# Performance work log

Measured on AMD Instinct MI355X. Metric: run time of the kernel, lower is better.

Reference implementation:

```python
import jax, jax.numpy as jnp
import numpy as np

N_CHEM = 100000
N_PROT = 20000
D = 128           # hidden_channels, also input feature dim (lazy SAGEConv)
E = 600000        # edges chem->protein (reverse relation uses flipped index)
EL = 200000       # label edges for decoder
L = 3             # SAGEConv layers


def setup_inputs() -> dict:
    key = jax.random.key(0)
    ks = jax.random.split(key, 11)
    inp = {
        'x_chem':    jax.random.normal(ks[0], (N_CHEM, D), jnp.float32),
        'x_protein': jax.random.normal(ks[1], (N_PROT, D), jnp.float32),
        # Wl/bl/Wr stacked over [layer, relation]; relation 0 = chem->protein (dst protein),
        # relation 1 = protein->chem (dst chem). PyG SAGEConv: lin_l has bias, lin_r does not.
        'Wl': jax.random.normal(ks[2], (L, 2, D, D), jnp.float32) * 0.05,
        'bl': jax.random.normal(ks[3], (L, 2, D), jnp.float32) * 0.05,
        'Wr': jax.random.normal(ks[4], (L, 2, D, D), jnp.float32) * 0.05,
        'Wd': jax.random.normal(ks[5], (1, 2 * D), jnp.float32) * 0.05,
        'bd': jax.random.normal(ks[6], (1,), jnp.float32) * 0.05,
        'src_idx': jax.random.randint(ks[7], (E,), 0, N_CHEM, jnp.int64),
        'dst_idx': jax.random.randint(ks[8], (E,), 0, N_PROT, jnp.int64),
        'row': jax.random.randint(ks[9], (EL,), 0, N_CHEM, jnp.int64),
        'col': jax.random.randint(ks[10], (EL,), 0, N_PROT, jnp.int64),
    }
    return inp


def _sage(x_src, x_dst, s_idx, d_idx, Wl, bl, Wr, n_dst):
    # PyG SAGEConv (aggr='mean'): lin_l(mean_j x_src[j]) + lin_r(x_dst)
    msg = x_src[s_idx]                                   # [E, D] gather
    agg = jax.ops.segment_sum(msg, d_idx, num_segments=n_dst)
    deg = jax.ops.segment_sum(jnp.ones((s_idx.shape[0],), x_src.dtype), d_idx,
                              num_segments=n_dst)
    mean = agg / jnp.clip(deg, 1.0)[:, None]
    return mean @ Wl.T + bl + x_dst @ Wr.T


def reference(x_chem, x_protein, Wl, bl, Wr, Wd, bd, src_idx, dst_idx, row, col):
    h_c, h_p = x_chem, x_protein
    for l in range(L):
        new_p = _sage(h_c, h_p, src_idx, dst_idx, Wl[l, 0], bl[l, 0], Wr[l, 0], N_PROT)
        new_c = _sage(h_p, h_c, dst_idx, src_idx, Wl[l, 1], bl[l, 1], Wr[l, 1], N_CHEM)
        h_c, h_p = jax.nn.relu(new_c), jax.nn.relu(new_p)
    # EdgeDecoder: gather + concat + linear -> flat scores
    x = jnp.concatenate([h_c[row], h_p[col]], axis=-1)   # [EL, 2D]
    z = (x @ Wd.T + bd).reshape(-1)                      # [EL]
    return (z, x)
```

## Files before the change

kernel.cpp:

```cpp
#include <hip/hip_runtime.h>

#define D128 128

typedef __attribute__((ext_vector_type(8))) short bf16x8;
typedef __attribute__((ext_vector_type(4))) float f32x4;
typedef unsigned short u16;
typedef unsigned int u32;

__device__ __forceinline__ u16 f2b(float f) {
  union { float f; u32 u; } x; x.f = f;
  u32 r = x.u + 0x7fffu + ((x.u >> 16) & 1u);
  return (u16)(r >> 16);
}
__device__ __forceinline__ float b2f(short s) {
  union { u32 u; float f; } x; x.u = ((u32)(unsigned short)s) << 16; return x.f;
}

#define GLD16(gp, lp) __builtin_amdgcn_global_load_lds( \
    (const __attribute__((address_space(1))) void*)(gp), \
    (__attribute__((address_space(3))) void*)(lp), 16, 0, 0)

__global__ __launch_bounds__(256) void cvt_deg_k(const float* __restrict__ xc, const float* __restrict__ xp,
                                                 const float* __restrict__ Wl, const float* __restrict__ Wr,
                                                 const int* __restrict__ src, const int* __restrict__ dst,
                                                 u16* __restrict__ B0, u16* __restrict__ Wcat,
                                                 int* __restrict__ deg, int NP, int NT, int E) {
  const int nqx = NT * 32;
  const int ncvt = nqx + 49152;
  const int TOT = ncvt + E;
  for (int i = blockIdx.x * 256 + threadIdx.x; i < TOT; i += gridDim.x * 256) {
    if (i < nqx) {
      const int r = i >> 5, c4 = (i & 31) << 2;
      const float* sp = (r < NP) ? &xp[(size_t)r * D128 + c4]
                                 : &xc[(size_t)(r - NP) * D128 + c4];
      float4 f = *(const float4*)sp;
      uint2 u;
      u.x = (u32)f2b(f.x) | ((u32)f2b(f.y) << 16);
      u.y = (u32)f2b(f.z) | ((u32)f2b(f.w) << 16);
      *(uint2*)&B0[(size_t)i * 4] = u;
    } else if (i < ncvt) {
      const int t = (i - nqx) * 4;
      const int slice = t >> 15, j = (t >> 8) & 127, k = t & 255;
      const float* sw = (k < 128) ? &Wl[(size_t)slice * 16384 + j * 128 + k]
                                  : &Wr[(size_t)slice * 16384 + j * 128 + (k - 128)];
      float4 f = *(const float4*)sw;
      uint2 u;
      u.x = (u32)f2b(f.x) | ((u32)f2b(f.y) << 16);
      u.y = (u32)f2b(f.z) | ((u32)f2b(f.w) << 16);
      *(uint2*)&Wcat[t] = u;
    } else {
      const int e = i - ncvt;
      atomicAdd(&deg[dst[e]], 1);
      atomicAdd(&deg[NP + src[e]], 1);
    }
  }
}

__global__ __launch_bounds__(256) void scan_k(const int* __restrict__ deg, int* __restrict__ offp, int NT) {
  __shared__ int sh[256];
  const int c = blockIdx.x;
  const int tid = threadIdx.x;
  int pre = 0;
  const int lim = c * 2048;
  for (int i = tid; i < lim; i += 256) pre += deg[i];
  sh[tid] = pre; __syncthreads();
#pragma unroll
  for (int o = 128; o > 0; o >>= 1) {
    if (tid < o) sh[tid] += sh[tid + o];
    __syncthreads();
  }
  const int base_pre = sh[0];
  __syncthreads();
  const int base = lim + tid * 8;
  int v[8]; int s = 0;
#pragma unroll
  for (int u = 0; u < 8; ++u) { int i = base + u; v[u] = (i < NT) ? deg[i] : 0; s += v[u]; }
  sh[tid] = s; __syncthreads();
#pragma unroll
  for (int o = 1; o < 256; o <<= 1) {
    int t = (tid >= o) ? sh[tid - o] : 0;
    __syncthreads();
    sh[tid] += t;
    __syncthreads();
  }
  int run = sh[tid] - s + base_pre;
#pragma unroll
  for (int u = 0; u < 8; ++u) { int i = base + u; if (i < NT) offp[i] = run; run += v[u]; }
}

__global__ __launch_bounds__(256) void fill_k(const int* __restrict__ src, const int* __restrict__ dst,
                                              const int* __restrict__ offp, int* cur, int* adj,
                                              int NP, int E) {
  int e = blockIdx.x * 256 + threadIdx.x;
  if (e >= E) return;
  const int s = src[e], d = dst[e];
  const int cn = NP + s;
  int pp = atomicAdd(&cur[d], 1);  adj[offp[d] + pp] = cn;
  int pc = atomicAdd(&cur[cn], 1); adj[offp[cn] + pc] = d;
}

__global__ __launch_bounds__(256) void agg_k(const u16* __restrict__ hcur, u16* __restrict__ hnext,
                                             const int* __restrict__ adj, const int* __restrict__ offp,
                                             const int* __restrict__ deg, int NT) {
  const int v = blockIdx.x * 16 + (threadIdx.x >> 4);
  if (v >= NT) return;
  const int l16 = threadIdx.x & 15;
  const int s = offp[v], cnt = deg[v];
  float ac[8] = {0.f, 0.f, 0.f, 0.f, 0.f, 0.f, 0.f, 0.f};
  int idx = (l16 < cnt) ? adj[s + l16] : 0;
  for (int n = 0; n < cnt; n += 16) {
    const int batch = (cnt - n < 16) ? (cnt - n) : 16;
    const int nrem = cnt - n - 16;
    const int idxn = (nrem > 0 && l16 < nrem) ? adj[s + n + 16 + l16] : 0;
    int j = 0;
    for (; j + 8 <= batch; j += 8) {
      int i0 = __shfl(idx, j, 16),     i1 = __shfl(idx, j + 1, 16);
      int i2 = __shfl(idx, j + 2, 16), i3 = __shfl(idx, j + 3, 16);
      int i4 = __shfl(idx, j + 4, 16), i5 = __shfl(idx, j + 5, 16);
      int i6 = __shfl(idx, j + 6, 16), i7 = __shfl(idx, j + 7, 16);
      bf16x8 r0 = *(const bf16x8*)&hcur[(size_t)i0 * D128 + l16 * 8];
      bf16x8 r1 = *(const bf16x8*)&hcur[(size_t)i1 * D128 + l16 * 8];
      bf16x8 r2 = *(const bf16x8*)&hcur[(size_t)i2 * D128 + l16 * 8];
      bf16x8 r3 = *(const bf16x8*)&hcur[(size_t)i3 * D128 + l16 * 8];
      bf16x8 r4 = *(const bf16x8*)&hcur[(size_t)i4 * D128 + l16 * 8];
      bf16x8 r5 = *(const bf16x8*)&hcur[(size_t)i5 * D128 + l16 * 8];
      bf16x8 r6 = *(const bf16x8*)&hcur[(size_t)i6 * D128 + l16 * 8];
      bf16x8 r7 = *(const bf16x8*)&hcur[(size_t)i7 * D128 + l16 * 8];
#pragma unroll
      for (int k = 0; k < 8; ++k)
        ac[k] += ((b2f(r0[k]) + b2f(r1[k])) + (b2f(r2[k]) + b2f(r3[k])))
               + ((b2f(r4[k]) + b2f(r5[k])) + (b2f(r6[k]) + b2f(r7[k])));
    }
    for (; j + 4 <= batch; j += 4) {
      int i0 = __shfl(idx, j, 16),     i1 = __shfl(idx, j + 1, 16);
      int i2 = __shfl(idx, j + 2, 16), i3 = __shfl(idx, j + 3, 16);
      bf16x8 r0 = *(const bf16x8*)&hcur[(size_t)i0 * D128 + l16 * 8];
      bf16x8 r1 = *(const bf16x8*)&hcur[(size_t)i1 * D128 + l16 * 8];
      bf16x8 r2 = *(const bf16x8*)&hcur[(size_t)i2 * D128 + l16 * 8];
      bf16x8 r3 = *(const bf16x8*)&hcur[(size_t)i3 * D128 + l16 * 8];
#pragma unroll
      for (int k = 0; k < 8; ++k)
        ac[k] += (b2f(r0[k]) + b2f(r1[k])) + (b2f(r2[k]) + b2f(r3[k]));
    }
    for (; j < batch; ++j) {
      int i0 = __shfl(idx, j, 16);
      bf16x8 r0 = *(const bf16x8*)&hcur[(size_t)i0 * D128 + l16 * 8];
#pragma unroll
      for (int k = 0; k < 8; ++k) ac[k] += b2f(r0[k]);
    }
    idx = idxn;
  }
  const float inv = (cnt > 0) ? 1.f / (float)cnt : 0.f;
  uint4 pk;
  pk.x = (u32)f2b(ac[0] * inv) | ((u32)f2b(ac[1] * inv) << 16);
  pk.y = (u32)f2b(ac[2] * inv) | ((u32)f2b(ac[3] * inv) << 16);
  pk.z = (u32)f2b(ac[4] * inv) | ((u32)f2b(ac[5] * inv) << 16);
  pk.w = (u32)f2b(ac[6] * inv) | ((u32)f2b(ac[7] * inv) << 16);
  *(uint4*)&hnext[(size_t)v * D128 + l16 * 8] = pk;
}

__global__ __launch_bounds__(256) void gemm_both_k(u16* __restrict__ hnext, const u16* __restrict__ hcur,
                                                   const u16* __restrict__ Wcat_l, const float* __restrict__ bl_l,
                                                   int NP, int NT, int tilesP) {
  __shared__ u16 As[128 * 64];
  __shared__ u16 Bs[128 * 64];
  const int t = blockIdx.x;
  const bool isP = t < tilesP;
  const int rbase = isP ? t * 128 : NP + (t - tilesP) * 128;
  const int hi = isP ? NP : NT;
  const u16* __restrict__ W = Wcat_l + (isP ? 0 : 32768);
  const float* __restrict__ bias = bl_l + (isP ? 0 : 128);

  const int tid = threadIdx.x;
  const int w = tid >> 6, lane = tid & 63;
  const int wr = w >> 1, wc = w & 1;
  const int l15 = lane & 15, chi = lane >> 4;

  f32x4 acc[4][4];
#pragma unroll
  for (int m = 0; m < 4; ++m)
#pragma unroll
    for (int n = 0; n < 4; ++n) acc[m][n] = (f32x4){0.f, 0.f, 0.f, 0.f};

  for (int ks = 0; ks < 4; ++ks) {
    const int k0 = ks * 64;
    const u16* Xsrc = (k0 < 128) ? hnext : hcur;
    const int kb = k0 & 127;
    if (ks) __syncthreads();
#pragma unroll
    for (int q = 0; q < 4; ++q) {
      const int ibase = w * 256 + q * 64;
      const int i = ibase + lane;
      const int r = i >> 3;
      const int cg = (i & 7) ^ (r & 7);
      int rr = rbase + r; if (rr >= hi) rr = hi - 1;
      GLD16(Xsrc + (size_t)rr * D128 + kb + cg * 8, (char*)As + ibase * 16);
      GLD16(W + (size_t)r * 256 + k0 + cg * 8, (char*)Bs + ibase * 16);
    }
    __syncthreads();
#pragma unroll
    for (int kk = 0; kk < 2; ++kk) {
      bf16x8 a[4], bfr[4];
      const int c = kk * 4 + chi;
#pragma unroll
      for (int m = 0; m < 4; ++m) {
        const int r = wr * 64 + m * 16 + l15;
        a[m] = *(const bf16x8*)((const char*)As + (r * 8 + (c ^ (r & 7))) * 16);
      }
#pragma unroll
      for (int n = 0; n < 4; ++n) {
        const int j = wc * 64 + n * 16 + l15;
        bfr[n] = *(const bf16x8*)((const char*)Bs + (j * 8 + (c ^ (j & 7))) * 16);
      }
#pragma unroll
      for (int m = 0; m < 4; ++m)
#pragma unroll
        for (int n = 0; n < 4; ++n)
          acc[m][n] = __builtin_amdgcn_mfma_f32_16x16x32_bf16(a[m], bfr[n], acc[m][n], 0, 0, 0);
    }
  }
#pragma unroll
  for (int n = 0; n < 4; ++n) {
    const int col = wc * 64 + n * 16 + l15;
    const float bv = bias[col];
#pragma unroll
    for (int m = 0; m < 4; ++m) {
      const int rb2 = rbase + wr * 64 + m * 16 + chi * 4;
#pragma unroll
      for (int q = 0; q < 4; ++q) {
        const int row = rb2 + q;
        if (row < hi) {
          float vv = acc[m][n][q] + bv;
          vv = vv > 0.f ? vv : 0.f;
          hnext[(size_t)row * D128 + col] = f2b(vv);
        }
      }
    }
  }
}

__global__ __launch_bounds__(256) void decoder_k(const u16* __restrict__ hf,
                                                 const int* __restrict__ rowi, const int* __restrict__ coli,
                                                 const float* __restrict__ Wd, const float* __restrict__ bd,
                                                 float* __restrict__ out, int NP, int EL) {
  typedef __attribute__((ext_vector_type(8))) unsigned short u16x8;
  const int lane = threadIdx.x & 63;
  const int half = lane >> 5;
  const int l32 = lane & 31;
  const int wid = blockIdx.x * 4 + (threadIdx.x >> 6);
  const int nw = gridDim.x * 4;
  float wvv[8];
#pragma unroll
  for (int k = 0; k < 8; ++k) wvv[k] = Wd[l32 * 8 + k];
  const float bdv = bd[0];
  for (int e = wid * 2 + half; e < EL; e += nw * 2) {
    const int r = rowi[e], c = coli[e];
    const size_t hrow = (l32 < 16) ? ((size_t)(NP + r) * D128 + l32 * 8)
                                   : ((size_t)c * D128 + (l32 - 16) * 8);
    const u16x8 hb = *(const u16x8*)&hf[hrow];
    float x0 = b2f((short)hb[0]), x1 = b2f((short)hb[1]);
    float x2 = b2f((short)hb[2]), x3 = b2f((short)hb[3]);
    float x4 = b2f((short)hb[4]), x5 = b2f((short)hb[5]);
    float x6 = b2f((short)hb[6]), x7 = b2f((short)hb[7]);
    float p = x0 * wvv[0] + x1 * wvv[1] + x2 * wvv[2] + x3 * wvv[3]
            + x4 * wvv[4] + x5 * wvv[5] + x6 * wvv[6] + x7 * wvv[7];
#pragma unroll
    for (int m = 1; m < 32; m <<= 1) p += __shfl_xor(p, m, 64);
    float* xo = out + (size_t)EL + (size_t)e * 256 + l32 * 8;
    f32x4 lo = {x0, x1, x2, x3};
    f32x4 hi2 = {x4, x5, x6, x7};
    __builtin_nontemporal_store(lo, (f32x4*)xo);
    __builtin_nontemporal_store(hi2, (f32x4*)(xo + 4));
    if (l32 == 0) __builtin_nontemporal_store(p + bdv, &out[e]);
  }
}


extern "C" void kernel_launch(void* const* d_in, const int* in_sizes, int n_in,
                              void* d_out, int out_size, void* d_ws, size_t ws_size,
                              hipStream_t stream) {
  const float* x_chem = (const float*)d_in[0];
  const float* x_prot = (const float*)d_in[1];
  const float* Wl = (const float*)d_in[2];
  const float* bl = (const float*)d_in[3];
  const float* Wr = (const float*)d_in[4];
  const float* Wd = (const float*)d_in[5];
  const float* bd = (const float*)d_in[6];
  const int* src = (const int*)d_in[7];
  const int* dst = (const int*)d_in[8];
  const int* row = (const int*)d_in[9];
  const int* col = (const int*)d_in[10];

  int NC = in_sizes[0] / D128;
  int NP = in_sizes[1] / D128;
  int E  = in_sizes[7];
  int EL = in_sizes[9];
  int NT = NP + NC;
  int nchunk = (NT + 2047) / 2048;
  float* out = (float*)d_out;

  char* w = (char*)d_ws;
  size_t szT = (size_t)NT * D128 * 2;
  u16* B0 = (u16*)w; w += szT;
  u16* B1 = (u16*)w; w += szT;
  u16* B2 = (u16*)w; w += szT;
  u16* Wcat = (u16*)w; w += (size_t)6 * 128 * 256 * 2;
  int* deg  = (int*)w; w += (size_t)NT * 4;
  int* cur  = (int*)w; w += (size_t)NT * 4;
  int* offp = (int*)w; w += (size_t)NT * 4;
  int* adj  = (int*)w; w += (size_t)2 * E * 4;
  if ((size_t)(w - (char*)d_ws) > ws_size) return;

  (void)hipMemsetAsync(deg, 0, (size_t)2 * NT * 4, stream);

  cvt_deg_k<<<2048, 256, 0, stream>>>(x_chem, x_prot, Wl, Wr, src, dst,
                                      B0, Wcat, deg, NP, NT, E);
  scan_k<<<nchunk, 256, 0, stream>>>(deg, offp, NT);
  fill_k<<<(E + 255) / 256, 256, 0, stream>>>(src, dst, offp, cur, adj, NP, E);

  const int tilesP = (NP + 127) >> 7;
  const int tilesC = (NC + 127) >> 7;
  u16* bufs[4] = {B0, B1, B2, B1};
  for (int l = 0; l < 3; ++l) {
    const u16* hcur = bufs[l];
    u16* hnext = bufs[l + 1];
    agg_k<<<(NT + 15) / 16, 256, 0, stream>>>(hcur, hnext, adj, offp, deg, NT);
    gemm_both_k<<<tilesP + tilesC, 256, 0, stream>>>(hnext, hcur,
                                                     Wcat + (size_t)l * 65536,
                                                     bl + (size_t)l * 256,
                                                     NP, NT, tilesP);
  }

  decoder_k<<<2048, 256, 0, stream>>>(B1, row, col, Wd, bd, out, NP, EL);
}
```

Before: 492.2 us.

## Split aggregation by feature slice with one node per thread

```diff
diff --git a/kernel.cpp b/kernel.cpp
--- a/kernel.cpp
+++ b/kernel.cpp
@@ -102,61 +102,41 @@
 __global__ __launch_bounds__(256) void agg_k(const u16* __restrict__ hcur, u16* __restrict__ hnext,
                                              const int* __restrict__ adj, const int* __restrict__ offp,
                                              const int* __restrict__ deg, int NT) {
-  const int v = blockIdx.x * 16 + (threadIdx.x >> 4);
-  if (v >= NT) return;
-  const int l16 = threadIdx.x & 15;
-  const int s = offp[v], cnt = deg[v];
-  float ac[8] = {0.f, 0.f, 0.f, 0.f, 0.f, 0.f, 0.f, 0.f};
-  int idx = (l16 < cnt) ? adj[s + l16] : 0;
-  for (int n = 0; n < cnt; n += 16) {
-    const int batch = (cnt - n < 16) ? (cnt - n) : 16;
-    const int nrem = cnt - n - 16;
-    const int idxn = (nrem > 0 && l16 < nrem) ? adj[s + n + 16 + l16] : 0;
-    int j = 0;
-    for (; j + 8 <= batch; j += 8) {
-      int i0 = __shfl(idx, j, 16),     i1 = __shfl(idx, j + 1, 16);
-      int i2 = __shfl(idx, j + 2, 16), i3 = __shfl(idx, j + 3, 16);
-      int i4 = __shfl(idx, j + 4, 16), i5 = __shfl(idx, j + 5, 16);
-      int i6 = __shfl(idx, j + 6, 16), i7 = __shfl(idx, j + 7, 16);
-      bf16x8 r0 = *(const bf16x8*)&hcur[(size_t)i0 * D128 + l16 * 8];
-      bf16x8 r1 = *(const bf16x8*)&hcur[(size_t)i1 * D128 + l16 * 8];
-      bf16x8 r2 = *(const bf16x8*)&hcur[(size_t)i2 * D128 + l16 * 8];
-      bf16x8 r3 = *(const bf16x8*)&hcur[(size_t)i3 * D128 + l16 * 8];
-      bf16x8 r4 = *(const bf16x8*)&hcur[(size_t)i4 * D128 + l16 * 8];
-      bf16x8 r5 = *(const bf16x8*)&hcur[(size_t)i5 * D128 + l16 * 8];
-      bf16x8 r6 = *(const bf16x8*)&hcur[(size_t)i6 * D128 + l16 * 8];
-      bf16x8 r7 = *(const bf16x8*)&hcur[(size_t)i7 * D128 + l16 * 8];
-#pragma unroll
-      for (int k = 0; k < 8; ++k)
-        ac[k] += ((b2f(r0[k]) + b2f(r1[k])) + (b2f(r2[k]) + b2f(r3[k])))
-               + ((b2f(r4[k]) + b2f(r5[k])) + (b2f(r6[k]) + b2f(r7[k])));
-    }
-    for (; j + 4 <= batch; j += 4) {
-      int i0 = __shfl(idx, j, 16),     i1 = __shfl(idx, j + 1, 16);
-      int i2 = __shfl(idx, j + 2, 16), i3 = __shfl(idx, j + 3, 16);
-      bf16x8 r0 = *(const bf16x8*)&hcur[(size_t)i0 * D128 + l16 * 8];
-      bf16x8 r1 = *(const bf16x8*)&hcur[(size_t)i1 * D128 + l16 * 8];
-      bf16x8 r2 = *(const bf16x8*)&hcur[(size_t)i2 * D128 + l16 * 8];
-      bf16x8 r3 = *(const bf16x8*)&hcur[(size_t)i3 * D128 + l16 * 8];
-#pragma unroll
-      for (int k = 0; k < 8; ++k)
-        ac[k] += (b2f(r0[k]) + b2f(r1[k])) + (b2f(r2[k]) + b2f(r3[k]));
-    }
-    for (; j < batch; ++j) {
-      int i0 = __shfl(idx, j, 16);
-      bf16x8 r0 = *(const bf16x8*)&hcur[(size_t)i0 * D128 + l16 * 8];
-#pragma unroll
-      for (int k = 0; k < 8; ++k) ac[k] += b2f(r0[k]);
-    }
-    idx = idxn;
-  }
-  const float inv = (cnt > 0) ? 1.f / (float)cnt : 0.f;
-  uint4 pk;
-  pk.x = (u32)f2b(ac[0] * inv) | ((u32)f2b(ac[1] * inv) << 16);
-  pk.y = (u32)f2b(ac[2] * inv) | ((u32)f2b(ac[3] * inv) << 16);
-  pk.z = (u32)f2b(ac[4] * inv) | ((u32)f2b(ac[5] * inv) << 16);
-  pk.w = (u32)f2b(ac[6] * inv) | ((u32)f2b(ac[7] * inv) << 16);
-  *(uint4*)&hnext[(size_t)v * D128 + l16 * 8] = pk;
+  const int s16 = (blockIdx.x & 7) * 16;
+  const int nch = gridDim.x >> 3;
+  const int tid = threadIdx.x;
+  for (int base = (blockIdx.x >> 3) * 256; base < NT; base += nch * 256) {
+    const int v = base + tid;
+    if (v < NT) {
+      const int so = offp[v], cnt = deg[v];
+      float ac[16];
+#pragma unroll
+      for (int k = 0; k < 16; ++k) ac[k] = 0.f;
+      int idx = (cnt > 0) ? adj[so] : 0;
+      for (int j = 0; j < cnt; ++j) {
+        const int nidx = (j + 1 < cnt) ? adj[so + j + 1] : 0;
+        const u16* rp = &hcur[(size_t)idx * D128 + s16];
+        bf16x8 r0 = *(const bf16x8*)rp;
+        bf16x8 r1 = *(const bf16x8*)(rp + 8);
+#pragma unroll
+        for (int k = 0; k < 8; ++k) { ac[k] += b2f(r0[k]); ac[8 + k] += b2f(r1[k]); }
+        idx = nidx;
+      }
+      const float inv = (cnt > 0) ? 1.f / (float)cnt : 0.f;
+      uint4 p0, p1;
+      p0.x = (u32)f2b(ac[0] * inv)  | ((u32)f2b(ac[1] * inv) << 16);
+      p0.y = (u32)f2b(ac[2] * inv)  | ((u32)f2b(ac[3] * inv) << 16);
+      p0.z = (u32)f2b(ac[4] * inv)  | ((u32)f2b(ac[5] * inv) << 16);
+      p0.w = (u32)f2b(ac[6] * inv)  | ((u32)f2b(ac[7] * inv) << 16);
+      p1.x = (u32)f2b(ac[8] * inv)  | ((u32)f2b(ac[9] * inv) << 16);
+      p1.y = (u32)f2b(ac[10] * inv) | ((u32)f2b(ac[11] * inv) << 16);
+      p1.z = (u32)f2b(ac[12] * inv) | ((u32)f2b(ac[13] * inv) << 16);
+      p1.w = (u32)f2b(ac[14] * inv) | ((u32)f2b(ac[15] * inv) << 16);
+      uint4* op = (uint4*)&hnext[(size_t)v * D128 + s16];
+      op[0] = p0;
+      op[1] = p1;
+    }
+  }
 }
 
 __global__ __launch_bounds__(256) void gemm_both_k(u16* __restrict__ hnext, const u16* __restrict__ hcur,
@@ -269,9 +249,9 @@
     float* xo = out + (size_t)EL + (size_t)e * 256 + l32 * 8;
     f32x4 lo = {x0, x1, x2, x3};
     f32x4 hi2 = {x4, x5, x6, x7};
-    __builtin_nontemporal_store(lo, (f32x4*)xo);
-    __builtin_nontemporal_store(hi2, (f32x4*)(xo + 4));
-    if (l32 == 0) __builtin_nontemporal_store(p + bdv, &out[e]);
+    *(f32x4*)xo = lo;
+    *(f32x4*)(xo + 4) = hi2;
+    if (l32 == 0) out[e] = p + bdv;
   }
 }
 
@@ -324,7 +304,7 @@
   for (int l = 0; l < 3; ++l) {
     const u16* hcur = bufs[l];
     u16* hnext = bufs[l + 1];
-    agg_k<<<(NT + 15) / 16, 256, 0, stream>>>(hcur, hnext, adj, offp, deg, NT);
+    agg_k<<<512, 256, 0, stream>>>(hcur, hnext, adj, offp, deg, NT);
     gemm_both_k<<<tilesP + tilesC, 256, 0, stream>>>(hnext, hcur,
                                                      Wcat + (size_t)l * 65536,
                                                      bl + (size_t)l * 256,
```

Result: slower. 886.2 us (+80.0%).

## Fuse neighbor mean aggregation into per-tile GEMM layer kernel via LDS

Applied to the files above, without the earlier changes.

```diff
diff --git a/kernel.cpp b/kernel.cpp
--- a/kernel.cpp
+++ b/kernel.cpp
@@ -15,10 +15,6 @@
 __device__ __forceinline__ float b2f(short s) {
   union { u32 u; float f; } x; x.u = ((u32)(unsigned short)s) << 16; return x.f;
 }
-
-#define GLD16(gp, lp) __builtin_amdgcn_global_load_lds( \
-    (const __attribute__((address_space(1))) void*)(gp), \
-    (__attribute__((address_space(3))) void*)(lp), 16, 0, 0)
 
 __global__ __launch_bounds__(256) void cvt_deg_k(const float* __restrict__ xc, const float* __restrict__ xp,
                                                  const float* __restrict__ Wl, const float* __restrict__ Wr,
@@ -99,140 +95,127 @@
   int pc = atomicAdd(&cur[cn], 1); adj[offp[cn] + pc] = d;
 }
 
-__global__ __launch_bounds__(256) void agg_k(const u16* __restrict__ hcur, u16* __restrict__ hnext,
-                                             const int* __restrict__ adj, const int* __restrict__ offp,
-                                             const int* __restrict__ deg, int NT) {
-  const int v = blockIdx.x * 16 + (threadIdx.x >> 4);
-  if (v >= NT) return;
-  const int l16 = threadIdx.x & 15;
-  const int s = offp[v], cnt = deg[v];
-  float ac[8] = {0.f, 0.f, 0.f, 0.f, 0.f, 0.f, 0.f, 0.f};
-  int idx = (l16 < cnt) ? adj[s + l16] : 0;
-  for (int n = 0; n < cnt; n += 16) {
-    const int batch = (cnt - n < 16) ? (cnt - n) : 16;
-    const int nrem = cnt - n - 16;
-    const int idxn = (nrem > 0 && l16 < nrem) ? adj[s + n + 16 + l16] : 0;
-    int j = 0;
-    for (; j + 8 <= batch; j += 8) {
-      int i0 = __shfl(idx, j, 16),     i1 = __shfl(idx, j + 1, 16);
-      int i2 = __shfl(idx, j + 2, 16), i3 = __shfl(idx, j + 3, 16);
-      int i4 = __shfl(idx, j + 4, 16), i5 = __shfl(idx, j + 5, 16);
-      int i6 = __shfl(idx, j + 6, 16), i7 = __shfl(idx, j + 7, 16);
-      bf16x8 r0 = *(const bf16x8*)&hcur[(size_t)i0 * D128 + l16 * 8];
-      bf16x8 r1 = *(const bf16x8*)&hcur[(size_t)i1 * D128 + l16 * 8];
-      bf16x8 r2 = *(const bf16x8*)&hcur[(size_t)i2 * D128 + l16 * 8];
-      bf16x8 r3 = *(const bf16x8*)&hcur[(size_t)i3 * D128 + l16 * 8];
-      bf16x8 r4 = *(const bf16x8*)&hcur[(size_t)i4 * D128 + l16 * 8];
-      bf16x8 r5 = *(const bf16x8*)&hcur[(size_t)i5 * D128 + l16 * 8];
-      bf16x8 r6 = *(const bf16x8*)&hcur[(size_t)i6 * D128 + l16 * 8];
-      bf16x8 r7 = *(const bf16x8*)&hcur[(size_t)i7 * D128 + l16 * 8];
-#pragma unroll
-      for (int k = 0; k < 8; ++k)
-        ac[k] += ((b2f(r0[k]) + b2f(r1[k])) + (b2f(r2[k]) + b2f(r3[k])))
-               + ((b2f(r4[k]) + b2f(r5[k])) + (b2f(r6[k]) + b2f(r7[k])));
-    }
-    for (; j + 4 <= batch; j += 4) {
-      int i0 = __shfl(idx, j, 16),     i1 = __shfl(idx, j + 1, 16);
-      int i2 = __shfl(idx, j + 2, 16), i3 = __shfl(idx, j + 3, 16);
-      bf16x8 r0 = *(const bf16x8*)&hcur[(size_t)i0 * D128 + l16 * 8];
-      bf16x8 r1 = *(const bf16x8*)&hcur[(size_t)i1 * D128 + l16 * 8];
-      bf16x8 r2 = *(const bf16x8*)&hcur[(size_t)i2 * D128 + l16 * 8];
-      bf16x8 r3 = *(const bf16x8*)&hcur[(size_t)i3 * D128 + l16 * 8];
-#pragma unroll
-      for (int k = 0; k < 8; ++k)
-        ac[k] += (b2f(r0[k]) + b2f(r1[k])) + (b2f(r2[k]) + b2f(r3[k]));
-    }
-    for (; j < batch; ++j) {
-      int i0 = __shfl(idx, j, 16);
-      bf16x8 r0 = *(const bf16x8*)&hcur[(size_t)i0 * D128 + l16 * 8];
-#pragma unroll
-      for (int k = 0; k < 8; ++k) ac[k] += b2f(r0[k]);
-    }
-    idx = idxn;
-  }
-  const float inv = (cnt > 0) ? 1.f / (float)cnt : 0.f;
-  uint4 pk;
-  pk.x = (u32)f2b(ac[0] * inv) | ((u32)f2b(ac[1] * inv) << 16);
-  pk.y = (u32)f2b(ac[2] * inv) | ((u32)f2b(ac[3] * inv) << 16);
-  pk.z = (u32)f2b(ac[4] * inv) | ((u32)f2b(ac[5] * inv) << 16);
-  pk.w = (u32)f2b(ac[6] * inv) | ((u32)f2b(ac[7] * inv) << 16);
-  *(uint4*)&hnext[(size_t)v * D128 + l16 * 8] = pk;
-}
-
-__global__ __launch_bounds__(256) void gemm_both_k(u16* __restrict__ hnext, const u16* __restrict__ hcur,
-                                                   const u16* __restrict__ Wcat_l, const float* __restrict__ bl_l,
-                                                   int NP, int NT, int tilesP) {
-  __shared__ u16 As[128 * 64];
-  __shared__ u16 Bs[128 * 64];
+__global__ __launch_bounds__(256) void layer_k(const u16* __restrict__ hcur, u16* __restrict__ hnext,
+                                               const int* __restrict__ adj, const int* __restrict__ offp,
+                                               const int* __restrict__ deg,
+                                               const u16* __restrict__ Wcat_l, const float* __restrict__ bl_l,
+                                               int NP, int NT, int tilesP) {
+  __shared__ u16 Am[128 * 128];
   const int t = blockIdx.x;
   const bool isP = t < tilesP;
   const int rbase = isP ? t * 128 : NP + (t - tilesP) * 128;
   const int hi = isP ? NP : NT;
   const u16* __restrict__ W = Wcat_l + (isP ? 0 : 32768);
   const float* __restrict__ bias = bl_l + (isP ? 0 : 128);
-
   const int tid = threadIdx.x;
-  const int w = tid >> 6, lane = tid & 63;
-  const int wr = w >> 1, wc = w & 1;
-  const int l15 = lane & 15, chi = lane >> 4;
-
-  f32x4 acc[4][4];
-#pragma unroll
-  for (int m = 0; m < 4; ++m)
-#pragma unroll
-    for (int n = 0; n < 4; ++n) acc[m][n] = (f32x4){0.f, 0.f, 0.f, 0.f};
-
-  for (int ks = 0; ks < 4; ++ks) {
-    const int k0 = ks * 64;
-    const u16* Xsrc = (k0 < 128) ? hnext : hcur;
-    const int kb = k0 & 127;
-    if (ks) __syncthreads();
-#pragma unroll
-    for (int q = 0; q < 4; ++q) {
-      const int ibase = w * 256 + q * 64;
-      const int i = ibase + lane;
-      const int r = i >> 3;
-      const int cg = (i & 7) ^ (r & 7);
-      int rr = rbase + r; if (rr >= hi) rr = hi - 1;
-      GLD16(Xsrc + (size_t)rr * D128 + kb + cg * 8, (char*)As + ibase * 16);
-      GLD16(W + (size_t)r * 256 + k0 + cg * 8, (char*)Bs + ibase * 16);
+
+  {
+    const int g = tid >> 4;
+    const int l16 = tid & 15;
+    const int half = l16 >> 3, cc = l16 & 7;
+    for (int rr = g * 8; rr < g * 8 + 8; ++rr) {
+      int v = rbase + rr; if (v >= hi) v = hi - 1;
+      const int so = offp[v], cnt = deg[v];
+      float ac[8] = {0.f, 0.f, 0.f, 0.f, 0.f, 0.f, 0.f, 0.f};
+      int j = 0;
+      for (; j + 8 <= cnt; j += 8) {
+        const int i0 = adj[so + j],     i1 = adj[so + j + 1];
+        const int i2 = adj[so + j + 2], i3 = adj[so + j + 3];
+        const int i4 = adj[so + j + 4], i5 = adj[so + j + 5];
+        const int i6 = adj[so + j + 6], i7 = adj[so + j + 7];
+        bf16x8 r0 = *(const bf16x8*)&hcur[(size_t)i0 * D128 + l16 * 8];
+        bf16x8 r1 = *(const bf16x8*)&hcur[(size_t)i1 * D128 + l16 * 8];
+        bf16x8 r2 = *(const bf16x8*)&hcur[(size_t)i2 * D128 + l16 * 8];
+        bf16x8 r3 = *(const bf16x8*)&hcur[(size_t)i3 * D128 + l16 * 8];
+        bf16x8 r4 = *(const bf16x8*)&hcur[(size_t)i4 * D128 + l16 * 8];
+        bf16x8 r5 = *(const bf16x8*)&hcur[(size_t)i5 * D128 + l16 * 8];
+        bf16x8 r6 = *(const bf16x8*)&hcur[(size_t)i6 * D128 + l16 * 8];
+        bf16x8 r7 = *(const bf16x8*)&hcur[(size_t)i7 * D128 + l16 * 8];
+#pragma unroll
+        for (int k = 0; k < 8; ++k)
+          ac[k] += ((b2f(r0[k]) + b2f(r1[k])) + (b2f(r2[k]) + b2f(r3[k])))
+                 + ((b2f(r4[k]) + b2f(r5[k])) + (b2f(r6[k]) + b2f(r7[k])));
+      }
+      for (; j + 4 <= cnt; j += 4) {
+        const int i0 = adj[so + j],     i1 = adj[so + j + 1];
+        const int i2 = adj[so + j + 2], i3 = adj[so + j + 3];
+        bf16x8 r0 = *(const bf16x8*)&hcur[(size_t)i0 * D128 + l16 * 8];
+        bf16x8 r1 = *(const bf16x8*)&hcur[(size_t)i1 * D128 + l16 * 8];
+        bf16x8 r2 = *(const bf16x8*)&hcur[(size_t)i2 * D128 + l16 * 8];
+        bf16x8 r3 = *(const bf16x8*)&hcur[(size_t)i3 * D128 + l16 * 8];
+#pragma unroll
+        for (int k = 0; k < 8; ++k)
+          ac[k] += (b2f(r0[k]) + b2f(r1[k])) + (b2f(r2[k]) + b2f(r3[k]));
+      }
+      for (; j < cnt; ++j) {
+        const int i0 = adj[so + j];
+        bf16x8 r0 = *(const bf16x8*)&hcur[(size_t)i0 * D128 + l16 * 8];
+#pragma unroll
+        for (int k = 0; k < 8; ++k) ac[k] += b2f(r0[k]);
+      }
+      const float inv = (cnt > 0) ? 1.f / (float)cnt : 0.f;
+      uint4 pk;
+      pk.x = (u32)f2b(ac[0] * inv) | ((u32)f2b(ac[1] * inv) << 16);
+      pk.y = (u32)f2b(ac[2] * inv) | ((u32)f2b(ac[3] * inv) << 16);
+      pk.z = (u32)f2b(ac[4] * inv) | ((u32)f2b(ac[5] * inv) << 16);
+      pk.w = (u32)f2b(ac[6] * inv) | ((u32)f2b(ac[7] * inv) << 16);
+      *(uint4*)&Am[rr * 128 + half * 64 + ((cc ^ (rr & 7)) << 3)] = pk;
     }
-    __syncthreads();
-#pragma unroll
-    for (int kk = 0; kk < 2; ++kk) {
-      bf16x8 a[4], bfr[4];
-      const int c = kk * 4 + chi;
+  }
+  __syncthreads();
+
+  {
+    const int w = tid >> 6, lane = tid & 63;
+    const int wr = w >> 1, wc = w & 1;
+    const int l15 = lane & 15, chi = lane >> 4;
+    f32x4 acc[4][4];
+#pragma unroll
+    for (int m = 0; m < 4; ++m)
+#pragma unroll
+      for (int n = 0; n < 4; ++n) acc[m][n] = (f32x4){0.f, 0.f, 0.f, 0.f};
+
+#pragma unroll
+    for (int ks = 0; ks < 4; ++ks) {
+#pragma unroll
+      for (int kk = 0; kk < 2; ++kk) {
+        bf16x8 a[4], bfr[4];
+#pragma unroll
+        for (int m = 0; m < 4; ++m) {
+          const int row = wr * 64 + m * 16 + l15;
+          if (ks < 2) {
+            a[m] = *(const bf16x8*)&Am[row * 128 + ks * 64 + (((kk * 4 + chi) ^ (row & 7)) << 3)];
+          } else {
+            int rg = rbase + row; if (rg >= hi) rg = hi - 1;
+            a[m] = *(const bf16x8*)&hcur[(size_t)rg * D128 + (ks - 2) * 64 + kk * 32 + chi * 8];
+          }
+        }
+#pragma unroll
+        for (int n = 0; n < 4; ++n) {
+          const int jc = wc * 64 + n * 16 + l15;
+          bfr[n] = *(const bf16x8*)&W[jc * 256 + ks * 64 + kk * 32 + chi * 8];
+        }
+#pragma unroll
+        for (int m = 0; m < 4; ++m)
+#pragma unroll
+          for (int n = 0; n < 4; ++n)
+            acc[m][n] = __builtin_amdgcn_mfma_f32_16x16x32_bf16(a[m], bfr[n], acc[m][n], 0, 0, 0);
+      }
+    }
+#pragma unroll
+    for (int n = 0; n < 4; ++n) {
+      const int col = wc * 64 + n * 16 + l15;
+      const float bv = bias[col];
 #pragma unroll
       for (int m = 0; m < 4; ++m) {
-        const int r = wr * 64 + m * 16 + l15;
-        a[m] = *(const bf16x8*)((const char*)As + (r * 8 + (c ^ (r & 7))) * 16);
-      }
-#pragma unroll
-      for (int n = 0; n < 4; ++n) {
-        const int j = wc * 64 + n * 16 + l15;
-        bfr[n] = *(const bf16x8*)((const char*)Bs + (j * 8 + (c ^ (j & 7))) * 16);
-      }
-#pragma unroll
-      for (int m = 0; m < 4; ++m)
-#pragma unroll
-        for (int n = 0; n < 4; ++n)
-          acc[m][n] = __builtin_amdgcn_mfma_f32_16x16x32_bf16(a[m], bfr[n], acc[m][n], 0, 0, 0);
-    }
-  }
-#pragma unroll
-  for (int n = 0; n < 4; ++n) {
-    const int col = wc * 64 + n * 16 + l15;
-    const float bv = bias[col];
-#pragma unroll
-    for (int m = 0; m < 4; ++m) {
-      const int rb2 = rbase + wr * 64 + m * 16 + chi * 4;
-#pragma unroll
-      for (int q = 0; q < 4; ++q) {
-        const int row = rb2 + q;
-        if (row < hi) {
-          float vv = acc[m][n][q] + bv;
-          vv = vv > 0.f ? vv : 0.f;
-          hnext[(size_t)row * D128 + col] = f2b(vv);
+        const int rb2 = rbase + wr * 64 + m * 16 + chi * 4;
+#pragma unroll
+        for (int q = 0; q < 4; ++q) {
+          const int row = rb2 + q;
+          if (row < hi) {
+            float vv = acc[m][n][q] + bv;
+            vv = vv > 0.f ? vv : 0.f;
+            hnext[(size_t)row * D128 + col] = f2b(vv);
+          }
         }
       }
     }
@@ -243,35 +226,24 @@
                                                  const int* __restrict__ rowi, const int* __restrict__ coli,
                                                  const float* __restrict__ Wd, const float* __restrict__ bd,
                                                  float* __restrict__ out, int NP, int EL) {
-  typedef __attribute__((ext_vector_type(8))) unsigned short u16x8;
   const int lane = threadIdx.x & 63;
-  const int half = lane >> 5;
-  const int l32 = lane & 31;
   const int wid = blockIdx.x * 4 + (threadIdx.x >> 6);
   const int nw = gridDim.x * 4;
-  float wvv[8];
-#pragma unroll
-  for (int k = 0; k < 8; ++k) wvv[k] = Wd[l32 * 8 + k];
+  const float4 wv = *(const float4*)&Wd[lane * 4];
   const float bdv = bd[0];
-  for (int e = wid * 2 + half; e < EL; e += nw * 2) {
+  for (int e = wid; e < EL; e += nw) {
     const int r = rowi[e], c = coli[e];
-    const size_t hrow = (l32 < 16) ? ((size_t)(NP + r) * D128 + l32 * 8)
-                                   : ((size_t)c * D128 + (l32 - 16) * 8);
-    const u16x8 hb = *(const u16x8*)&hf[hrow];
-    float x0 = b2f((short)hb[0]), x1 = b2f((short)hb[1]);
-    float x2 = b2f((short)hb[2]), x3 = b2f((short)hb[3]);
-    float x4 = b2f((short)hb[4]), x5 = b2f((short)hb[5]);
-    float x6 = b2f((short)hb[6]), x7 = b2f((short)hb[7]);
-    float p = x0 * wvv[0] + x1 * wvv[1] + x2 * wvv[2] + x3 * wvv[3]
-            + x4 * wvv[4] + x5 * wvv[5] + x6 * wvv[6] + x7 * wvv[7];
-#pragma unroll
-    for (int m = 1; m < 32; m <<= 1) p += __shfl_xor(p, m, 64);
-    float* xo = out + (size_t)EL + (size_t)e * 256 + l32 * 8;
-    f32x4 lo = {x0, x1, x2, x3};
-    f32x4 hi2 = {x4, x5, x6, x7};
-    __builtin_nontemporal_store(lo, (f32x4*)xo);
-    __builtin_nontemporal_store(hi2, (f32x4*)(xo + 4));
-    if (l32 == 0) __builtin_nontemporal_store(p + bdv, &out[e]);
+    const u16* hrow = (lane < 32) ? &hf[(size_t)(NP + r) * D128 + lane * 4]
+                                  : &hf[(size_t)c * D128 + (lane * 4 - 128)];
+    const ushort4 hb = *(const ushort4*)hrow;
+    const float x0 = b2f((short)hb.x), x1 = b2f((short)hb.y);
+    const float x2 = b2f((short)hb.z), x3 = b2f((short)hb.w);
+    float p = x0 * wv.x + x1 * wv.y + x2 * wv.z + x3 * wv.w;
+#pragma unroll
+    for (int m = 1; m < 64; m <<= 1) p += __shfl_xor(p, m, 64);
+    f32x4 st = {x0, x1, x2, x3};
+    *(f32x4*)&out[(size_t)EL + (size_t)e * 256 + lane * 4] = st;
+    if (lane == 0) out[e] = p + bdv;
   }
 }
 
@@ -322,13 +294,10 @@
   const int tilesC = (NC + 127) >> 7;
   u16* bufs[4] = {B0, B1, B2, B1};
   for (int l = 0; l < 3; ++l) {
-    const u16* hcur = bufs[l];
-    u16* hnext = bufs[l + 1];
-    agg_k<<<(NT + 15) / 16, 256, 0, stream>>>(hcur, hnext, adj, offp, deg, NT);
-    gemm_both_k<<<tilesP + tilesC, 256, 0, stream>>>(hnext, hcur,
-                                                     Wcat + (size_t)l * 65536,
-                                                     bl + (size_t)l * 256,
-                                                     NP, NT, tilesP);
+    layer_k<<<tilesP + tilesC, 256, 0, stream>>>(bufs[l], bufs[l + 1], adj, offp, deg,
+                                                 Wcat + (size_t)l * 65536,
+                                                 bl + (size_t)l * 256,
+                                                 NP, NT, tilesP);
   }
 
   decoder_k<<<2048, 256, 0, stream>>>(B1, row, col, Wd, bd, out, NP, EL);
```

New measurement: 625.4 us. +27.1%, slower.
